# Kernel tuning notes

Measured on AMD Instinct MI355X. Metric: run time of the kernel, lower is better.

The kernel has to match this reference:

```python
import jax, jax.numpy as jnp
import numpy as np

B, T, H, A, E, V = 32, 128, 1024, 1024, 512, 512  # A==H required by the module's cat/Linear shapes


def setup_inputs() -> dict:
    key = jax.random.key(0)
    ks = jax.random.split(key, 13)
    s = 0.02
    return {
        "encoder_outputs": jax.random.normal(ks[0], (B, A, E), jnp.float32),
        "hidden": jax.random.normal(ks[1], (1, B, H), jnp.float32),
        "target_seq": jax.random.normal(ks[2], (B, T, H), jnp.float32),
        "W_att": jax.random.normal(ks[3], (H + A, A), jnp.float32) * s,
        "b_att": jax.random.normal(ks[4], (A,), jnp.float32) * s,
        "W_comb": jax.random.normal(ks[5], (H + E, H), jnp.float32) * s,
        "b_comb": jax.random.normal(ks[6], (H,), jnp.float32) * s,
        "W_ih": jax.random.normal(ks[7], (3 * H, H), jnp.float32) * s,
        "b_ih": jax.random.normal(ks[8], (3 * H,), jnp.float32) * s,
        "W_hh": jax.random.normal(ks[9], (3 * H, H), jnp.float32) * s,
        "b_hh": jax.random.normal(ks[10], (3 * H,), jnp.float32) * s,
        "W_out": jax.random.normal(ks[11], (H, V), jnp.float32) * s,
        "b_out": jax.random.normal(ks[12], (V,), jnp.float32) * s,
    }


def reference(encoder_outputs, hidden, target_seq, W_att, b_att, W_comb, b_comb,
              W_ih, b_ih, W_hh, b_hh, W_out, b_out):
    # Teacher forcing: decoder input at step t is zeros (t=0) then target_seq[:, t-1]
    dec_in = jnp.concatenate([jnp.zeros_like(target_seq[:, :1]), target_seq[:, :-1]], axis=1)  # [B,T,H]
    dec_ts = jnp.swapaxes(dec_in, 0, 1)  # [T,B,H]

    def step(h, dec):  # h: [B,H], dec: [B,H]
        # attention over encoder positions (softmax width A == encoder seq len)
        attn = jax.nn.softmax(jnp.concatenate([dec, h], axis=1) @ W_att + b_att, axis=1)  # [B,A]
        ctx = jnp.einsum('bl,ble->be', attn, encoder_outputs)  # [B,E]
        g = jax.nn.relu(jnp.concatenate([dec, ctx], axis=1) @ W_comb + b_comb)  # [B,H]
        # GRU cell (torch gate order r, z, n)
        gi = g @ W_ih.T + b_ih
        gh = h @ W_hh.T + b_hh
        ir, iz, i_n = jnp.split(gi, 3, axis=1)
        hr, hz, h_n = jnp.split(gh, 3, axis=1)
        r = jax.nn.sigmoid(ir + hr)
        z = jax.nn.sigmoid(iz + hz)
        n = jnp.tanh(i_n + r * h_n)
        h_new = (1.0 - z) * n + z * h
        out_tok = h_new @ W_out + b_out  # [B,V]
        return h_new, out_tok

    h_last, outs = jax.lax.scan(step, hidden[0], dec_ts)  # outs: [T,B,V]
    output_seq = jnp.swapaxes(outs, 0, 1)  # [B,T,V]
    return output_seq, h_last[None]
```

## Files before the change

kernel.cpp:

```cpp
#include <hip/hip_runtime.h>

typedef unsigned short u16;
typedef unsigned int u32;
typedef unsigned long long u64;
typedef short v8s __attribute__((ext_vector_type(8)));
typedef float v4f __attribute__((ext_vector_type(4)));
typedef int v4i __attribute__((ext_vector_type(4)));

#define MFMA16(a, b, c) __builtin_amdgcn_mfma_f32_16x16x32_bf16((a), (b), (c), 0, 0, 0)

#define B_ 32
#define T_ 128
#define H_ 1024
#define A_ 1024
#define E_ 512
#define V_ 512
#define NBLK 256
#define NTH 512
#define NSLOT 32
#define AGGB 248
#define ENC_LDS_BYTES 131072
#define SCRATCH_BYTES 28672
#define DSMEM_BYTES (ENC_LDS_BYTES + SCRATCH_BYTES)

__device__ __forceinline__ float b2f(u16 u) {
  union { u32 u; float f; } c; c.u = ((u32)u) << 16; return c.f;
}
__device__ __forceinline__ u16 f2b(float f) {
  union { float f; u32 u; } c; c.f = f;
  u32 x = c.u;
  x += 0x7fffu + ((x >> 16) & 1u);
  return (u16)(x >> 16);
}

__device__ __forceinline__ void ato_st(u32* p, u32 v) {
  __hip_atomic_store(p, v, __ATOMIC_RELAXED, __HIP_MEMORY_SCOPE_AGENT);
}
__device__ __forceinline__ void ato_stf(float* p, float v) {
  union { float f; u32 u; } c; c.f = v; ato_st((u32*)p, c.u);
}
__device__ __forceinline__ void ato_addf(float* p, float v) {
  __hip_atomic_fetch_add(p, v, __ATOMIC_RELAXED, __HIP_MEMORY_SCOPE_AGENT);
}

__device__ __forceinline__ v4i ld16_sc1(const void* p) {
  v4i r;
  asm volatile("global_load_dwordx4 %0, %1, off sc1" : "=v"(r) : "v"(p));
  return r;
}
__device__ __forceinline__ float ld4_sc1(const void* p) {
  float r;
  asm volatile("global_load_dword %0, %1, off sc1" : "=v"(r) : "v"(p));
  return r;
}
__device__ __forceinline__ void wait_vm0() {
  asm volatile("s_waitcnt vmcnt(0)" ::: "memory");
  __builtin_amdgcn_sched_barrier(0);
}
__device__ __forceinline__ v8s as8(v4i x) { union { v4i a; v8s b; } u; u.a = x; return u.b; }
__device__ __forceinline__ void cvt8(v4i qa, v4i qb, v8s& hi, v8s& lo) {
  union { v4i q; float f[4]; } a, b;
  a.q = qa; b.q = qb;
  float v[8] = {a.f[0], a.f[1], a.f[2], a.f[3], b.f[0], b.f[1], b.f[2], b.f[3]};
  u16 hh[8], ll[8];
  #pragma unroll
  for (int i = 0; i < 8; ++i) {
    float x = fmaxf(v[i], 0.f);
    u16 hv = f2b(x);
    hh[i] = hv; ll[i] = f2b(x - b2f(hv));
  }
  hi = *(v8s*)hh; lo = *(v8s*)ll;
}

__device__ __forceinline__ void grid_bar(u32* arr, u32 ep) {
  u32* lvl2 = arr + NBLK * NSLOT;
  asm volatile("s_waitcnt vmcnt(0)" ::: "memory");
  __syncthreads();
  if (threadIdx.x == 0)
    __hip_atomic_store(arr + blockIdx.x * NSLOT, ep, __ATOMIC_RELAXED, __HIP_MEMORY_SCOPE_AGENT);
  if (blockIdx.x >= AGGB) {
    int g = blockIdx.x - AGGB;
    if (threadIdx.x < 32) {
      while (__hip_atomic_load(arr + (g * 32 + threadIdx.x) * NSLOT,
                               __ATOMIC_RELAXED, __HIP_MEMORY_SCOPE_AGENT) < ep)
        __builtin_amdgcn_s_sleep(1);
    }
    if (threadIdx.x == 0)
      __hip_atomic_store(lvl2 + g, ep, __ATOMIC_RELAXED, __HIP_MEMORY_SCOPE_AGENT);
  }
  if (threadIdx.x < 8) {
    while (__hip_atomic_load(lvl2 + threadIdx.x, __ATOMIC_RELAXED, __HIP_MEMORY_SCOPE_AGENT) < ep)
      __builtin_amdgcn_s_sleep(1);
  }
  __syncthreads();
  asm volatile("" ::: "memory");
}

__device__ __forceinline__ void gemm_nk(const u16* ah, const u16* al, size_t mstr,
                                        const u16* bp, int nk, v4f& c0, v4f& c1) {
  #pragma unroll 2
  for (int i = 0; i < nk; ++i) {
    v8s b   = *(const v8s*)(bp);
    v8s a0h = *(const v8s*)(ah);
    v8s a1h = *(const v8s*)(ah + mstr);
    v8s a0l = *(const v8s*)(al);
    v8s a1l = *(const v8s*)(al + mstr);
    c0 = MFMA16(a0h, b, c0);
    c1 = MFMA16(a1h, b, c1);
    c0 = MFMA16(a0l, b, c0);
    c1 = MFMA16(a1l, b, c1);
    ah += 32; al += 32; bp += 32;
  }
}

__device__ __forceinline__ void red_store2(float* part, int wv, int lane, v4f c0, v4f c1) {
  float* p = part + (wv * 64 + lane) * 8;
  #pragma unroll
  for (int r = 0; r < 4; ++r) { p[r] = c0[r]; p[4 + r] = c1[r]; }
}
__device__ __forceinline__ float red_sum2(const float* part, int o) {
  int m = o >> 4, n = o & 15;
  int lane = (((m & 15) >> 2) << 4) + n;
  int idx = ((m >> 4) << 2) + (m & 3);
  float s = 0.f;
  #pragma unroll
  for (int w = 0; w < 8; ++w) s += part[(w * 64 + lane) * 8 + idx];
  return s;
}

__global__ void __launch_bounds__(NTH, 1)
dec_persist(const u16* __restrict__ WattT, const u16* __restrict__ Whh_b,
            const u16* __restrict__ Wih_b, const u16* __restrict__ Wc_ctxT,
            const float* __restrict__ enc_f,
            const float* __restrict__ bih, const float* __restrict__ bhh,
            const float* __restrict__ ldec_all,
            float* h, float* logit, float* gh, float* g_all,
            u16* hbf_hi, u16* hbf_lo, u16* hseqb, u32* bar)
{
  const int tid = threadIdx.x;
  const int bid = blockIdx.x;
  const int lane = tid & 63;
  const int wv = tid >> 6;
  const int ln = lane & 15;
  const int kq8 = (lane >> 4) * 8;

  extern __shared__ __align__(16) unsigned char dsm[];
  u16* lds_enc = (u16*)dsm;
  float* scratch = (float*)(dsm + ENC_LDS_BYTES);

  {
    int b = bid >> 3, e0 = (bid & 7) * 64;
    const float* src = enc_f + (size_t)b * A_ * E_ + e0 + (tid & 7) * 8;
    int seg = (tid & 7) * 8;
    for (int i = 0; i < 16; ++i) {
      int row = i * 64 + (tid >> 3);
      const float* sp = src + (size_t)row * E_;
      float4 a = *(const float4*)sp;
      float4 bq = *(const float4*)(sp + 4);
      u16 tmp[8] = {f2b(a.x), f2b(a.y), f2b(a.z), f2b(a.w),
                    f2b(bq.x), f2b(bq.y), f2b(bq.z), f2b(bq.w)};
      *(v8s*)(lds_enc + row * 64 + seg) = *(v8s*)tmp;
    }
  }

  u32 ep = 0;

  for (int t = 0; t < T_; ++t) {
    {
      float* part = scratch;
      size_t a0 = (size_t)ln * H_ + wv * 128 + kq8;
      v4i ah0[4], ah1[4], al0[4], al1[4];
      #pragma unroll
      for (int i = 0; i < 4; ++i) {
        ah0[i] = ld16_sc1(hbf_hi + a0 + i * 32);
        ah1[i] = ld16_sc1(hbf_hi + a0 + 16 * H_ + i * 32);
        al0[i] = ld16_sc1(hbf_lo + a0 + i * 32);
        al1[i] = ld16_sc1(hbf_lo + a0 + 16 * H_ + i * 32);
      }
      float ldec = 0.f;
      const u16* bp;
      int n0;
      if (bid < 64) {
        n0 = bid * 16;
        ldec = ldec_all[(size_t)t * (B_ * A_) + (tid >> 4) * A_ + n0 + (tid & 15)];
        bp = WattT + (size_t)(n0 + ln) * 2048 + 1024 + wv * 128 + kq8;
      } else {
        n0 = (bid - 64) * 16;
        bp = Whh_b + (size_t)(n0 + ln) * H_ + wv * 128 + kq8;
      }
      v8s wb[4];
      #pragma unroll
      for (int i = 0; i < 4; ++i) wb[i] = *(const v8s*)(bp + i * 32);
      v4f c0 = {0.f, 0.f, 0.f, 0.f}, c1 = {0.f, 0.f, 0.f, 0.f};
      wait_vm0();
      #pragma unroll
      for (int i = 0; i < 4; ++i) {
        c0 = MFMA16(as8(ah0[i]), wb[i], c0);
        c1 = MFMA16(as8(ah1[i]), wb[i], c1);
        c0 = MFMA16(as8(al0[i]), wb[i], c0);
        c1 = MFMA16(as8(al1[i]), wb[i], c1);
      }
      red_store2(part, wv, lane, c0, c1);
      __syncthreads();
      {
        float s = red_sum2(part, tid);
        int m = tid >> 4, n = tid & 15;
        if (bid < 64) {
          ato_stf(&logit[m * A_ + n0 + n], s + ldec);
        } else {
          ato_stf(&gh[(size_t)(n0 + n) * 32 + m], s + bhh[n0 + n]);
        }
      }
    }
    grid_bar(bar, ++ep);

    {
      float* p    = scratch;
      float* part = scratch + 1024;
      float* red  = scratch + 5120;
      float* sctx = scratch + 5136;
      int b = bid >> 3, es = bid & 7;
      float v1 = ld4_sc1(&logit[b * A_ + tid]);
      float v2 = ld4_sc1(&logit[b * A_ + 512 + tid]);
      wait_vm0();
      float mx = fmaxf(v1, v2);
      #pragma unroll
      for (int off = 32; off; off >>= 1) mx = fmaxf(mx, __shfl_xor(mx, off));
      if (lane == 0) red[wv] = mx;
      __syncthreads();
      float mfull = red[0];
      #pragma unroll
      for (int q = 1; q < 8; ++q) mfull = fmaxf(mfull, red[q]);
      float e1 = __expf(v1 - mfull), e2 = __expf(v2 - mfull);
      p[tid] = e1; p[512 + tid] = e2;
      float sm = e1 + e2;
      #pragma unroll
      for (int off = 32; off; off >>= 1) sm += __shfl_xor(sm, off);
      if (lane == 0) red[8 + wv] = sm;
      __syncthreads();
      float ssum = red[8];
      #pragma unroll
      for (int q = 1; q < 8; ++q) ssum += red[8 + q];
      float inv = 1.f / ssum;

      int le = lane & 7, lr = lane >> 3;
      float acc[8] = {0.f, 0.f, 0.f, 0.f, 0.f, 0.f, 0.f, 0.f};
      #pragma unroll 4
      for (int i = 0; i < 16; ++i) {
        int l = i * 64 + wv * 8 + lr;
        v8s w = *(const v8s*)(lds_enc + l * 64 + le * 8);
        float pv = p[l];
        #pragma unroll
        for (int r = 0; r < 8; ++r) acc[r] += pv * b2f((u16)w[r]);
      }
      float* pp = part + ((wv * 8 + lr) * 8 + le) * 8;
      #pragma unroll
      for (int r = 0; r < 8; ++r) pp[r] = acc[r];
      __syncthreads();
      if (tid < 64) {
        int eo = tid >> 3, r = tid & 7;
        float s = 0.f;
        #pragma unroll
        for (int q = 0; q < 64; ++q) s += part[q * 64 + eo * 8 + r];
        sctx[tid] = s * inv;
      }
      __syncthreads();
      {
        const u16* w0 = Wc_ctxT + (size_t)(2 * tid) * E_ + es * 64;
        const u16* w1 = w0 + E_;
        float a0 = 0.f, a1 = 0.f;
        #pragma unroll
        for (int i = 0; i < 8; ++i) {
          v8s q0 = *(const v8s*)(w0 + i * 8);
          v8s q1 = *(const v8s*)(w1 + i * 8);
          #pragma unroll
          for (int r = 0; r < 8; ++r) {
            float pv = sctx[i * 8 + r];
            a0 += pv * b2f((u16)q0[r]);
            a1 += pv * b2f((u16)q1[r]);
          }
        }
        float* gp = g_all + (size_t)t * (B_ * H_) + b * H_ + 2 * tid;
        ato_addf(gp, a0);
        ato_addf(gp + 1, a1);
      }
    }
    grid_bar(bar, ++ep);

    {
      if (bid < 64) {
        float* part = scratch;
        float* hx   = scratch + 6144;
        int j0 = bid * 16;
        const float* gbase = g_all + (size_t)t * (B_ * H_);
        int koff0 = wv * 128 + kq8;
        v4i gr0[8], gr1[8];
        #pragma unroll
        for (int i = 0; i < 4; ++i) {
          const float* p0 = gbase + (size_t)ln * H_ + koff0 + i * 32;
          const float* p1 = gbase + (size_t)(ln + 16) * H_ + koff0 + i * 32;
          gr0[2 * i]     = ld16_sc1(p0);
          gr0[2 * i + 1] = ld16_sc1(p0 + 4);
          gr1[2 * i]     = ld16_sc1(p1);
          gr1[2 * i + 1] = ld16_sc1(p1 + 4);
        }
        const u16* bp0 = Wih_b + (size_t)(j0 + ln) * H_ + koff0;
        const u16* bp1 = bp0 + (size_t)H_ * H_;
        const u16* bp2 = bp0 + (size_t)2 * H_ * H_;
        v8s wb0[4], wb1[4], wb2[4];
        #pragma unroll
        for (int i = 0; i < 4; ++i) {
          wb0[i] = *(const v8s*)(bp0 + i * 32);
          wb1[i] = *(const v8s*)(bp1 + i * 32);
          wb2[i] = *(const v8s*)(bp2 + i * 32);
        }
        v4f c00 = {0.f,0.f,0.f,0.f}, c01 = c00, c02 = c00, c10 = c00, c11 = c00, c12 = c00;
        wait_vm0();
        #pragma unroll
        for (int i = 0; i < 4; ++i) {
          v8s a0h, a0l, a1h, a1l;
          cvt8(gr0[2 * i], gr0[2 * i + 1], a0h, a0l);
          cvt8(gr1[2 * i], gr1[2 * i + 1], a1h, a1l);
          c00 = MFMA16(a0h, wb0[i], c00); c00 = MFMA16(a0l, wb0[i], c00);
          c01 = MFMA16(a0h, wb1[i], c01); c01 = MFMA16(a0l, wb1[i], c01);
          c02 = MFMA16(a0h, wb2[i], c02); c02 = MFMA16(a0l, wb2[i], c02);
          c10 = MFMA16(a1h, wb0[i], c10); c10 = MFMA16(a1l, wb0[i], c10);
          c11 = MFMA16(a1h, wb1[i], c11); c11 = MFMA16(a1l, wb1[i], c11);
          c12 = MFMA16(a1h, wb2[i], c12); c12 = MFMA16(a1l, wb2[i], c12);
        }
        float hr0 = 0.f, hz0 = 0.f, hn0 = 0.f, hr1 = 0.f, hz1 = 0.f, hn1 = 0.f;
        float ho0 = 0.f, ho1 = 0.f;
        int obl = tid >> 4, jj = tid & 15, j = j0 + jj;
        if (tid < 256) {
          hr0 = ld4_sc1(&gh[(size_t)j * 32 + obl]);
          hz0 = ld4_sc1(&gh[(size_t)(H_ + j) * 32 + obl]);
          hn0 = ld4_sc1(&gh[(size_t)(2 * H_ + j) * 32 + obl]);
          hr1 = ld4_sc1(&gh[(size_t)j * 32 + 16 + obl]);
          hz1 = ld4_sc1(&gh[(size_t)(H_ + j) * 32 + 16 + obl]);
          hn1 = ld4_sc1(&gh[(size_t)(2 * H_ + j) * 32 + 16 + obl]);
          ho0 = h[obl * H_ + j];
          ho1 = h[(obl + 16) * H_ + j];
        }
        float bi_r = 0.f, bi_z = 0.f, bi_n = 0.f;
        if (tid < 256) {
          bi_r = bih[j]; bi_z = bih[H_ + j]; bi_n = bih[2 * H_ + j];
        }
        #pragma unroll
        for (int pass = 0; pass < 2; ++pass) {
          float* pp = part + (wv * 64 + lane) * 12;
          if (pass == 0) {
            #pragma unroll
            for (int r = 0; r < 4; ++r) { pp[r] = c00[r]; pp[4 + r] = c01[r]; pp[8 + r] = c02[r]; }
          } else {
            #pragma unroll
            for (int r = 0; r < 4; ++r) { pp[r] = c10[r]; pp[4 + r] = c11[r]; pp[8 + r] = c12[r]; }
          }
          __syncthreads();
          if (tid < 256) {
            if (pass == 0) wait_vm0();
            int ob = pass * 16 + obl;
            int lanei = ((obl >> 2) << 4) + jj;
            int rg = obl & 3;
            float ir = 0.f, iz = 0.f, in_ = 0.f;
            #pragma unroll
            for (int w = 0; w < 8; ++w) {
              const float* q = part + (w * 64 + lanei) * 12;
              ir += q[rg]; iz += q[4 + rg]; in_ += q[8 + rg];
            }
            ir += bi_r; iz += bi_z; in_ += bi_n;
            float hr = pass ? hr1 : hr0;
            float hz = pass ? hz1 : hz0;
            float hn = pass ? hn1 : hn0;
            float ho = pass ? ho1 : ho0;
            float r = 1.f / (1.f + __expf(-(ir + hr)));
            float z = 1.f / (1.f + __expf(-(iz + hz)));
            float n = tanhf(in_ + r * hn);
            float hnew = (1.f - z) * n + z * ho;
            h[ob * H_ + j] = hnew;
            hx[ob * 16 + jj] = hnew;
          }
          __syncthreads();
        }
        if (tid < 256) {
          int ob2 = tid >> 3, j2 = (tid & 7) * 2;
          float v0 = hx[ob2 * 16 + j2], v1 = hx[ob2 * 16 + j2 + 1];
          u16 h0 = f2b(v0), h1 = f2b(v1);
          u16 l0 = f2b(v0 - b2f(h0)), l1 = f2b(v1 - b2f(h1));
          int idx = ob2 * H_ + j0 + j2;
          u32 hp = (u32)h0 | ((u32)h1 << 16);
          ato_st((u32*)(hbf_hi + idx), hp);
          ato_st((u32*)(hbf_lo + idx), (u32)l0 | ((u32)l1 << 16));
          *(u32*)(hseqb + ((size_t)t * 32 + ob2) * H_ + j0 + j2) = hp;
        }
      }
    }
    grid_bar(bar, ++ep);
  }
}

__global__ void __launch_bounds__(256)
dec_gemm(const u16* __restrict__ th, const u16* __restrict__ tl,
         const u16* __restrict__ W, const unsigned long wstride,
         const float* __restrict__ bias, float* __restrict__ out)
{
  int tid = threadIdx.x, lane = tid & 63, wv = tid >> 6;
  int ln = lane & 15, kq8 = (lane >> 4) * 8;
  int t = blockIdx.x >> 4, nt = blockIdx.x & 15;
  float* op = out + (size_t)t * (32 * 1024);
  if (t == 0) {
    for (int i = tid; i < 32 * 64; i += 256) {
      int b = i >> 6, n = nt * 64 + (i & 63);
      op[(size_t)b * 1024 + n] = bias[n];
    }
    return;
  }
  int n0w = nt * 64 + wv * 16;
  const u16* ah = th + ((size_t)ln * T_ + (t - 1)) * H_ + kq8;
  const u16* al = tl + ((size_t)ln * T_ + (t - 1)) * H_ + kq8;
  const u16* bp = W + (size_t)(n0w + ln) * wstride + kq8;
  v4f c0 = {0.f, 0.f, 0.f, 0.f}, c1 = {0.f, 0.f, 0.f, 0.f};
  gemm_nk(ah, al, (size_t)16 * T_ * H_, bp, 32, c0, c1);
  int n = n0w + (lane & 15);
  float bo = bias[n];
  int rb = (lane >> 4) * 4;
  #pragma unroll
  for (int r = 0; r < 4; ++r) {
    op[(size_t)(rb + r) * 1024 + n] = c0[r] + bo;
    op[(size_t)(rb + r + 16) * 1024 + n] = c1[r] + bo;
  }
}

__global__ void __launch_bounds__(256, 2)
out_gemm(const u16* __restrict__ hseqb, const u16* __restrict__ WoutT,
         const float* __restrict__ bout, float* __restrict__ out)
{
  int tid = threadIdx.x, lane = tid & 63, wv = tid >> 6;
  int ln = lane & 15, kq8 = (lane >> 4) * 8;
  int m0 = (blockIdx.x >> 3) * 32;
  int n0 = (blockIdx.x & 7) * 64 + wv * 16;
  v4f c0 = {0.f, 0.f, 0.f, 0.f}, c1 = {0.f, 0.f, 0.f, 0.f};
  const u16* ap = hseqb + (size_t)(m0 + ln) * 1024 + kq8;
  const u16* bp = WoutT + (size_t)(n0 + ln) * 1024 + kq8;
  for (int i = 0; i < 32; ++i) {
    v8s b = *(const v8s*)bp;
    v8s a0 = *(const v8s*)ap;
    v8s a1 = *(const v8s*)(ap + 16 * 1024);
    c0 = MFMA16(a0, b, c0);
    c1 = MFMA16(a1, b, c1);
    ap += 32; bp += 32;
  }
  int v = n0 + ln;
  float bo = bout[v];
  int rbase = (lane >> 4) * 4;
  #pragma unroll
  for (int rg = 0; rg < 4; ++rg) {
    int m = m0 + rbase + rg;
    out[((size_t)(m & 31) * T_ + (m >> 5)) * V_ + v] = c0[rg] + bo;
    int m2 = m + 16;
    out[((size_t)(m2 & 31) * T_ + (m2 >> 5)) * V_ + v] = c1[rg] + bo;
  }
}

__global__ void __launch_bounds__(256)
hlast_copy(const float* __restrict__ h, float* __restrict__ out)
{
  int i = blockIdx.x * 256 + threadIdx.x;
  if (i < B_ * H_) out[(size_t)B_ * T_ * V_ + i] = h[i];
}

__global__ void __launch_bounds__(256)
k_cvt(const float* __restrict__ in, u16* __restrict__ out, int n)
{
  int stride = gridDim.x * 256;
  for (int i = blockIdx.x * 256 + threadIdx.x; i < n; i += stride) out[i] = f2b(in[i]);
}

__global__ void __launch_bounds__(256)
k_cvt_split(const float* __restrict__ in, u16* __restrict__ hi, u16* __restrict__ lo, int n)
{
  int stride = gridDim.x * 256;
  for (int i = blockIdx.x * 256 + threadIdx.x; i < n; i += stride) {
    float x = in[i];
    u16 a = f2b(x);
    hi[i] = a;
    lo[i] = f2b(x - b2f(a));
  }
}

__global__ void __launch_bounds__(256)
k_tr(const float* __restrict__ in, u16* __restrict__ out, int R, int C)
{
  __shared__ float tile[32][33];
  int tc = C >> 5;
  int r0 = (blockIdx.x / tc) << 5, c0 = (blockIdx.x % tc) << 5;
  int tx = threadIdx.x & 31, ty = threadIdx.x >> 5;
  #pragma unroll
  for (int q = 0; q < 4; ++q) {
    int r = ty + q * 8;
    tile[r][tx] = in[(size_t)(r0 + r) * C + c0 + tx];
  }
  __syncthreads();
  #pragma unroll
  for (int q = 0; q < 4; ++q) {
    int r = ty + q * 8;
    out[(size_t)(c0 + r) * R + r0 + tx] = f2b(tile[tx][r]);
  }
}

__global__ void __launch_bounds__(256)
k_init(const float* __restrict__ hidden, float* h, u16* hhi, u16* hlo)
{
  int i = blockIdx.x * 256 + threadIdx.x;
  if (i < B_ * H_) {
    float x = hidden[i];
    h[i] = x;
    u16 a = f2b(x);
    hhi[i] = a;
    hlo[i] = f2b(x - b2f(a));
  }
}

extern "C" void kernel_launch(void* const* d_in, const int* in_sizes, int n_in,
                              void* d_out, int out_size, void* d_ws, size_t ws_size,
                              hipStream_t stream) {
  (void)in_sizes; (void)n_in; (void)out_size; (void)ws_size;
  const float* enc    = (const float*)d_in[0];
  const float* hidden = (const float*)d_in[1];
  const float* tgt    = (const float*)d_in[2];
  const float* Watt   = (const float*)d_in[3];
  const float* batt   = (const float*)d_in[4];
  const float* Wcomb  = (const float*)d_in[5];
  const float* bcomb  = (const float*)d_in[6];
  const float* Wih    = (const float*)d_in[7];
  const float* bih    = (const float*)d_in[8];
  const float* Whh    = (const float*)d_in[9];
  const float* bhh    = (const float*)d_in[10];
  const float* Wout   = (const float*)d_in[11];
  const float* bout   = (const float*)d_in[12];

  size_t off = 0;
  char* base = (char*)d_ws;
  auto alloc = [&](size_t bytes) -> void* {
    void* p = base + off;
    off += (bytes + 255) & ~(size_t)255;
    return p;
  };
  size_t bar_bytes = (size_t)(NBLK * NSLOT + 64) * 4;
  u32*   bar    = (u32*)  alloc(bar_bytes);
  float* h      = (float*)alloc(B_ * H_ * 4);
  float* logit  = (float*)alloc(B_ * A_ * 4);
  float* gh     = (float*)alloc((size_t)3 * H_ * B_ * 4);
  float* ldec_all = (float*)alloc((size_t)T_ * B_ * A_ * 4);
  float* g_all    = (float*)alloc((size_t)T_ * B_ * H_ * 4);
  u16*   hbf_hi = (u16*)  alloc(B_ * H_ * 2);
  u16*   hbf_lo = (u16*)  alloc(B_ * H_ * 2);
  u16*   hseqb  = (u16*)  alloc((size_t)T_ * B_ * H_ * 2);
  u16*   tgt_hi = (u16*)  alloc((size_t)B_ * T_ * H_ * 2);
  u16*   tgt_lo = (u16*)  alloc((size_t)B_ * T_ * H_ * 2);
  u16*   WattT  = (u16*)  alloc((size_t)2048 * 1024 * 2);
  u16*   Whh_b  = (u16*)  alloc((size_t)3 * H_ * H_ * 2);
  u16*   Wih_b  = (u16*)  alloc((size_t)3 * H_ * H_ * 2);
  u16*   WcombT = (u16*)  alloc((size_t)1024 * 1536 * 2);
  u16*   Wc_ctxT= (u16*)  alloc((size_t)1024 * 512 * 2);
  u16*   WoutT  = (u16*)  alloc((size_t)512 * 1024 * 2);

  hipMemsetAsync(bar, 0, bar_bytes, stream);

  k_cvt_split<<<2048, 256, 0, stream>>>(tgt, tgt_hi, tgt_lo, B_ * T_ * H_);
  k_cvt<<<2048, 256, 0, stream>>>(Whh, Whh_b, 3 * H_ * H_);
  k_cvt<<<2048, 256, 0, stream>>>(Wih, Wih_b, 3 * H_ * H_);
  k_tr<<<64 * 32, 256, 0, stream>>>(Watt, WattT, 2048, 1024);
  k_tr<<<48 * 32, 256, 0, stream>>>(Wcomb, WcombT, 1536, 1024);
  k_tr<<<16 * 32, 256, 0, stream>>>(Wcomb + (size_t)1024 * H_, Wc_ctxT, 512, 1024);
  k_tr<<<32 * 16, 256, 0, stream>>>(Wout, WoutT, 1024, 512);
  k_init<<<128, 256, 0, stream>>>(hidden, h, hbf_hi, hbf_lo);

  dec_gemm<<<2048, 256, 0, stream>>>(tgt_hi, tgt_lo, WattT, 2048UL, batt, ldec_all);
  dec_gemm<<<2048, 256, 0, stream>>>(tgt_hi, tgt_lo, WcombT, 1536UL, bcomb, g_all);

  hipFuncSetAttribute((const void*)dec_persist,
                      hipFuncAttributeMaxDynamicSharedMemorySize, DSMEM_BYTES);

  dec_persist<<<NBLK, NTH, DSMEM_BYTES, stream>>>(WattT, Whh_b, Wih_b, Wc_ctxT, enc,
                                                  bih, bhh, ldec_all,
                                                  h, logit, gh, g_all,
                                                  hbf_hi, hbf_lo, hseqb, bar);
  out_gemm<<<1024, 256, 0, stream>>>(hseqb, WoutT, bout, (float*)d_out);
  hlast_copy<<<128, 256, 0, stream>>>(h, (float*)d_out);
}
```

Before: 4.405 ms.

## Use per-step hidden-state history with plain loads and a flat grid barrier

The single overwritten bf16 hidden buffer becomes a (T+1)-deep history. Each step therefore reads fresh addresses, so the sc1 cache-bypass loads and explicit vmcnt waits are dropped in favour of ordinary vector loads, with weight loads interleaved into the MFMA loop. The history buffer also feeds the output GEMM directly, which removes the separate hseqb store. The two-level aggregated grid barrier is replaced by a flat one in which each block polls all 256 block slots. This cuts one barrier hop per sync but adds more polling traffic, and plain loads of g_all risk reading stale cached data across XCDs.

```diff
diff --git a/kernel.cpp b/kernel.cpp
--- a/kernel.cpp
+++ b/kernel.cpp
@@ -5,7 +5,6 @@
 typedef unsigned long long u64;
 typedef short v8s __attribute__((ext_vector_type(8)));
 typedef float v4f __attribute__((ext_vector_type(4)));
-typedef int v4i __attribute__((ext_vector_type(4)));
 
 #define MFMA16(a, b, c) __builtin_amdgcn_mfma_f32_16x16x32_bf16((a), (b), (c), 0, 0, 0)
 
@@ -18,7 +17,6 @@
 #define NBLK 256
 #define NTH 512
 #define NSLOT 32
-#define AGGB 248
 #define ENC_LDS_BYTES 131072
 #define SCRATCH_BYTES 28672
 #define DSMEM_BYTES (ENC_LDS_BYTES + SCRATCH_BYTES)
@@ -43,11 +41,6 @@
   __hip_atomic_fetch_add(p, v, __ATOMIC_RELAXED, __HIP_MEMORY_SCOPE_AGENT);
 }
 
-__device__ __forceinline__ v4i ld16_sc1(const void* p) {
-  v4i r;
-  asm volatile("global_load_dwordx4 %0, %1, off sc1" : "=v"(r) : "v"(p));
-  return r;
-}
 __device__ __forceinline__ float ld4_sc1(const void* p) {
   float r;
   asm volatile("global_load_dword %0, %1, off sc1" : "=v"(r) : "v"(p));
@@ -57,11 +50,8 @@
   asm volatile("s_waitcnt vmcnt(0)" ::: "memory");
   __builtin_amdgcn_sched_barrier(0);
 }
-__device__ __forceinline__ v8s as8(v4i x) { union { v4i a; v8s b; } u; u.a = x; return u.b; }
-__device__ __forceinline__ void cvt8(v4i qa, v4i qb, v8s& hi, v8s& lo) {
-  union { v4i q; float f[4]; } a, b;
-  a.q = qa; b.q = qb;
-  float v[8] = {a.f[0], a.f[1], a.f[2], a.f[3], b.f[0], b.f[1], b.f[2], b.f[3]};
+__device__ __forceinline__ void cvt8f(float4 qa, float4 qb, v8s& hi, v8s& lo) {
+  float v[8] = {qa.x, qa.y, qa.z, qa.w, qb.x, qb.y, qb.z, qb.w};
   u16 hh[8], ll[8];
   #pragma unroll
   for (int i = 0; i < 8; ++i) {
@@ -73,23 +63,12 @@
 }
 
 __device__ __forceinline__ void grid_bar(u32* arr, u32 ep) {
-  u32* lvl2 = arr + NBLK * NSLOT;
   asm volatile("s_waitcnt vmcnt(0)" ::: "memory");
   __syncthreads();
   if (threadIdx.x == 0)
     __hip_atomic_store(arr + blockIdx.x * NSLOT, ep, __ATOMIC_RELAXED, __HIP_MEMORY_SCOPE_AGENT);
-  if (blockIdx.x >= AGGB) {
-    int g = blockIdx.x - AGGB;
-    if (threadIdx.x < 32) {
-      while (__hip_atomic_load(arr + (g * 32 + threadIdx.x) * NSLOT,
-                               __ATOMIC_RELAXED, __HIP_MEMORY_SCOPE_AGENT) < ep)
-        __builtin_amdgcn_s_sleep(1);
-    }
-    if (threadIdx.x == 0)
-      __hip_atomic_store(lvl2 + g, ep, __ATOMIC_RELAXED, __HIP_MEMORY_SCOPE_AGENT);
-  }
-  if (threadIdx.x < 8) {
-    while (__hip_atomic_load(lvl2 + threadIdx.x, __ATOMIC_RELAXED, __HIP_MEMORY_SCOPE_AGENT) < ep)
+  if (threadIdx.x < NBLK) {
+    while (__hip_atomic_load(arr + threadIdx.x * NSLOT, __ATOMIC_RELAXED, __HIP_MEMORY_SCOPE_AGENT) < ep)
       __builtin_amdgcn_s_sleep(1);
   }
   __syncthreads();
@@ -135,7 +114,7 @@
             const float* __restrict__ bih, const float* __restrict__ bhh,
             const float* __restrict__ ldec_all,
             float* h, float* logit, float* gh, float* g_all,
-            u16* hbf_hi, u16* hbf_lo, u16* hseqb, u32* bar)
+            u16* hs_hi, u16* hs_lo, u32* bar)
 {
   const int tid = threadIdx.x;
   const int bid = blockIdx.x;
@@ -168,14 +147,16 @@
   for (int t = 0; t < T_; ++t) {
     {
       float* part = scratch;
+      const u16* hb = hs_hi + (size_t)t * (B_ * H_);
+      const u16* lb = hs_lo + (size_t)t * (B_ * H_);
       size_t a0 = (size_t)ln * H_ + wv * 128 + kq8;
-      v4i ah0[4], ah1[4], al0[4], al1[4];
+      v8s ah0[4], ah1[4], al0[4], al1[4];
       #pragma unroll
       for (int i = 0; i < 4; ++i) {
-        ah0[i] = ld16_sc1(hbf_hi + a0 + i * 32);
-        ah1[i] = ld16_sc1(hbf_hi + a0 + 16 * H_ + i * 32);
-        al0[i] = ld16_sc1(hbf_lo + a0 + i * 32);
-        al1[i] = ld16_sc1(hbf_lo + a0 + 16 * H_ + i * 32);
+        ah0[i] = *(const v8s*)(hb + a0 + i * 32);
+        ah1[i] = *(const v8s*)(hb + a0 + 16 * H_ + i * 32);
+        al0[i] = *(const v8s*)(lb + a0 + i * 32);
+        al1[i] = *(const v8s*)(lb + a0 + 16 * H_ + i * 32);
       }
       float ldec = 0.f;
       const u16* bp;
@@ -188,17 +169,14 @@
         n0 = (bid - 64) * 16;
         bp = Whh_b + (size_t)(n0 + ln) * H_ + wv * 128 + kq8;
       }
-      v8s wb[4];
-      #pragma unroll
-      for (int i = 0; i < 4; ++i) wb[i] = *(const v8s*)(bp + i * 32);
       v4f c0 = {0.f, 0.f, 0.f, 0.f}, c1 = {0.f, 0.f, 0.f, 0.f};
-      wait_vm0();
       #pragma unroll
       for (int i = 0; i < 4; ++i) {
-        c0 = MFMA16(as8(ah0[i]), wb[i], c0);
-        c1 = MFMA16(as8(ah1[i]), wb[i], c1);
-        c0 = MFMA16(as8(al0[i]), wb[i], c0);
-        c1 = MFMA16(as8(al1[i]), wb[i], c1);
+        v8s wb = *(const v8s*)(bp + i * 32);
+        c0 = MFMA16(ah0[i], wb, c0);
+        c1 = MFMA16(ah1[i], wb, c1);
+        c0 = MFMA16(al0[i], wb, c0);
+        c1 = MFMA16(al1[i], wb, c1);
       }
       red_store2(part, wv, lane, c0, c1);
       __syncthreads();
@@ -294,39 +272,32 @@
         int j0 = bid * 16;
         const float* gbase = g_all + (size_t)t * (B_ * H_);
         int koff0 = wv * 128 + kq8;
-        v4i gr0[8], gr1[8];
+        float4 ga[4][2], gb[4][2];
         #pragma unroll
         for (int i = 0; i < 4; ++i) {
           const float* p0 = gbase + (size_t)ln * H_ + koff0 + i * 32;
           const float* p1 = gbase + (size_t)(ln + 16) * H_ + koff0 + i * 32;
-          gr0[2 * i]     = ld16_sc1(p0);
-          gr0[2 * i + 1] = ld16_sc1(p0 + 4);
-          gr1[2 * i]     = ld16_sc1(p1);
-          gr1[2 * i + 1] = ld16_sc1(p1 + 4);
+          ga[i][0] = *(const float4*)p0; ga[i][1] = *(const float4*)(p0 + 4);
+          gb[i][0] = *(const float4*)p1; gb[i][1] = *(const float4*)(p1 + 4);
         }
         const u16* bp0 = Wih_b + (size_t)(j0 + ln) * H_ + koff0;
         const u16* bp1 = bp0 + (size_t)H_ * H_;
         const u16* bp2 = bp0 + (size_t)2 * H_ * H_;
-        v8s wb0[4], wb1[4], wb2[4];
+        v4f c00 = {0.f,0.f,0.f,0.f}, c01 = c00, c02 = c00, c10 = c00, c11 = c00, c12 = c00;
         #pragma unroll
         for (int i = 0; i < 4; ++i) {
-          wb0[i] = *(const v8s*)(bp0 + i * 32);
-          wb1[i] = *(const v8s*)(bp1 + i * 32);
-          wb2[i] = *(const v8s*)(bp2 + i * 32);
-        }
-        v4f c00 = {0.f,0.f,0.f,0.f}, c01 = c00, c02 = c00, c10 = c00, c11 = c00, c12 = c00;
-        wait_vm0();
-        #pragma unroll
-        for (int i = 0; i < 4; ++i) {
+          v8s wb0 = *(const v8s*)(bp0 + i * 32);
+          v8s wb1 = *(const v8s*)(bp1 + i * 32);
+          v8s wb2 = *(const v8s*)(bp2 + i * 32);
           v8s a0h, a0l, a1h, a1l;
-          cvt8(gr0[2 * i], gr0[2 * i + 1], a0h, a0l);
-          cvt8(gr1[2 * i], gr1[2 * i + 1], a1h, a1l);
-          c00 = MFMA16(a0h, wb0[i], c00); c00 = MFMA16(a0l, wb0[i], c00);
-          c01 = MFMA16(a0h, wb1[i], c01); c01 = MFMA16(a0l, wb1[i], c01);
-          c02 = MFMA16(a0h, wb2[i], c02); c02 = MFMA16(a0l, wb2[i], c02);
-          c10 = MFMA16(a1h, wb0[i], c10); c10 = MFMA16(a1l, wb0[i], c10);
-          c11 = MFMA16(a1h, wb1[i], c11); c11 = MFMA16(a1l, wb1[i], c11);
-          c12 = MFMA16(a1h, wb2[i], c12); c12 = MFMA16(a1l, wb2[i], c12);
+          cvt8f(ga[i][0], ga[i][1], a0h, a0l);
+          cvt8f(gb[i][0], gb[i][1], a1h, a1l);
+          c00 = MFMA16(a0h, wb0, c00); c00 = MFMA16(a0l, wb0, c00);
+          c01 = MFMA16(a0h, wb1, c01); c01 = MFMA16(a0l, wb1, c01);
+          c02 = MFMA16(a0h, wb2, c02); c02 = MFMA16(a0l, wb2, c02);
+          c10 = MFMA16(a1h, wb0, c10); c10 = MFMA16(a1l, wb0, c10);
+          c11 = MFMA16(a1h, wb1, c11); c11 = MFMA16(a1l, wb1, c11);
+          c12 = MFMA16(a1h, wb2, c12); c12 = MFMA16(a1l, wb2, c12);
         }
         float hr0 = 0.f, hz0 = 0.f, hn0 = 0.f, hr1 = 0.f, hz1 = 0.f, hn1 = 0.f;
         float ho0 = 0.f, ho1 = 0.f;
@@ -386,11 +357,9 @@
           float v0 = hx[ob2 * 16 + j2], v1 = hx[ob2 * 16 + j2 + 1];
           u16 h0 = f2b(v0), h1 = f2b(v1);
           u16 l0 = f2b(v0 - b2f(h0)), l1 = f2b(v1 - b2f(h1));
-          int idx = ob2 * H_ + j0 + j2;
-          u32 hp = (u32)h0 | ((u32)h1 << 16);
-          ato_st((u32*)(hbf_hi + idx), hp);
-          ato_st((u32*)(hbf_lo + idx), (u32)l0 | ((u32)l1 << 16));
-          *(u32*)(hseqb + ((size_t)t * 32 + ob2) * H_ + j0 + j2) = hp;
+          size_t idx = (size_t)(t + 1) * (B_ * H_) + ob2 * H_ + j0 + j2;
+          ato_st((u32*)(hs_hi + idx), (u32)h0 | ((u32)h1 << 16));
+          ato_st((u32*)(hs_lo + idx), (u32)l0 | ((u32)l1 << 16));
         }
       }
     }
@@ -410,7 +379,7 @@
   if (t == 0) {
     for (int i = tid; i < 32 * 64; i += 256) {
       int b = i >> 6, n = nt * 64 + (i & 63);
-      op[(size_t)b * 1024 + n] = bias[n];
+      ato_stf(&op[(size_t)b * 1024 + n], bias[n]);
     }
     return;
   }
@@ -425,13 +394,13 @@
   int rb = (lane >> 4) * 4;
   #pragma unroll
   for (int r = 0; r < 4; ++r) {
-    op[(size_t)(rb + r) * 1024 + n] = c0[r] + bo;
-    op[(size_t)(rb + r + 16) * 1024 + n] = c1[r] + bo;
+    ato_stf(&op[(size_t)(rb + r) * 1024 + n], c0[r] + bo);
+    ato_stf(&op[(size_t)(rb + r + 16) * 1024 + n], c1[r] + bo);
   }
 }
 
 __global__ void __launch_bounds__(256, 2)
-out_gemm(const u16* __restrict__ hseqb, const u16* __restrict__ WoutT,
+out_gemm(const u16* __restrict__ hseq, const u16* __restrict__ WoutT,
          const float* __restrict__ bout, float* __restrict__ out)
 {
   int tid = threadIdx.x, lane = tid & 63, wv = tid >> 6;
@@ -439,7 +408,7 @@
   int m0 = (blockIdx.x >> 3) * 32;
   int n0 = (blockIdx.x & 7) * 64 + wv * 16;
   v4f c0 = {0.f, 0.f, 0.f, 0.f}, c1 = {0.f, 0.f, 0.f, 0.f};
-  const u16* ap = hseqb + (size_t)(m0 + ln) * 1024 + kq8;
+  const u16* ap = hseq + (size_t)(m0 + ln) * 1024 + kq8;
   const u16* bp = WoutT + (size_t)(n0 + ln) * 1024 + kq8;
   for (int i = 0; i < 32; ++i) {
     v8s b = *(const v8s*)bp;
@@ -508,15 +477,15 @@
 }
 
 __global__ void __launch_bounds__(256)
-k_init(const float* __restrict__ hidden, float* h, u16* hhi, u16* hlo)
+k_init(const float* __restrict__ hidden, float* h, u16* hs_hi, u16* hs_lo)
 {
   int i = blockIdx.x * 256 + threadIdx.x;
   if (i < B_ * H_) {
     float x = hidden[i];
     h[i] = x;
     u16 a = f2b(x);
-    hhi[i] = a;
-    hlo[i] = f2b(x - b2f(a));
+    hs_hi[i] = a;
+    hs_lo[i] = f2b(x - b2f(a));
   }
 }
 
@@ -552,9 +521,8 @@
   float* gh     = (float*)alloc((size_t)3 * H_ * B_ * 4);
   float* ldec_all = (float*)alloc((size_t)T_ * B_ * A_ * 4);
   float* g_all    = (float*)alloc((size_t)T_ * B_ * H_ * 4);
-  u16*   hbf_hi = (u16*)  alloc(B_ * H_ * 2);
-  u16*   hbf_lo = (u16*)  alloc(B_ * H_ * 2);
-  u16*   hseqb  = (u16*)  alloc((size_t)T_ * B_ * H_ * 2);
+  u16*   hs_hi  = (u16*)  alloc((size_t)(T_ + 1) * B_ * H_ * 2);
+  u16*   hs_lo  = (u16*)  alloc((size_t)(T_ + 1) * B_ * H_ * 2);
   u16*   tgt_hi = (u16*)  alloc((size_t)B_ * T_ * H_ * 2);
   u16*   tgt_lo = (u16*)  alloc((size_t)B_ * T_ * H_ * 2);
   u16*   WattT  = (u16*)  alloc((size_t)2048 * 1024 * 2);
@@ -573,7 +541,7 @@
   k_tr<<<48 * 32, 256, 0, stream>>>(Wcomb, WcombT, 1536, 1024);
   k_tr<<<16 * 32, 256, 0, stream>>>(Wcomb + (size_t)1024 * H_, Wc_ctxT, 512, 1024);
   k_tr<<<32 * 16, 256, 0, stream>>>(Wout, WoutT, 1024, 512);
-  k_init<<<128, 256, 0, stream>>>(hidden, h, hbf_hi, hbf_lo);
+  k_init<<<128, 256, 0, stream>>>(hidden, h, hs_hi, hs_lo);
 
   dec_gemm<<<2048, 256, 0, stream>>>(tgt_hi, tgt_lo, WattT, 2048UL, batt, ldec_all);
   dec_gemm<<<2048, 256, 0, stream>>>(tgt_hi, tgt_lo, WcombT, 1536UL, bcomb, g_all);
@@ -584,7 +552,7 @@
   dec_persist<<<NBLK, NTH, DSMEM_BYTES, stream>>>(WattT, Whh_b, Wih_b, Wc_ctxT, enc,
                                                   bih, bhh, ldec_all,
                                                   h, logit, gh, g_all,
-                                                  hbf_hi, hbf_lo, hseqb, bar);
-  out_gemm<<<1024, 256, 0, stream>>>(hseqb, WoutT, bout, (float*)d_out);
+                                                  hs_hi, hs_lo, bar);
+  out_gemm<<<1024, 256, 0, stream>>>(hs_hi + B_ * H_, WoutT, bout, (float*)d_out);
   hlast_copy<<<128, 256, 0, stream>>>(h, (float*)d_out);
 }
```

Result: faster. 4.164 ms (-5.5%).
